# Performance work log

Hardware: AMD Instinct MI355X
Metric: run time of the kernel (lower is better)

Reference implementation:

```python
import jax, jax.numpy as jnp
import numpy as np

BS, RAL, LAL = 128, 1024, 256
CS, VOC, HFS, EMB = 256, 34, 512, 256


def setup_inputs() -> dict:
    key0 = jax.random.key(0)
    ks = jax.random.split(key0, 16)
    s = 0.02
    # mask from random valid lengths (at least 1 valid frame per example)
    lengths = jax.random.randint(ks[15], (BS,), RAL // 2, RAL + 1)
    mask = (jnp.arange(RAL)[None, :] < lengths[:, None]).astype(jnp.float32)
    return {
        "key": jax.random.normal(ks[0], (BS, RAL, CS), jnp.float32),
        "val": jax.random.normal(ks[1], (BS, RAL, CS), jnp.float32),
        "mask": mask,
        "emb": jax.random.normal(ks[2], (VOC, EMB), jnp.float32) * s,
        "Wih_a": jax.random.normal(ks[3], (4 * HFS, EMB + CS), jnp.float32) * s,
        "Whh_a": jax.random.normal(ks[4], (4 * HFS, HFS), jnp.float32) * s,
        "bih_a": jnp.zeros((4 * HFS,), jnp.float32),
        "bhh_a": jnp.zeros((4 * HFS,), jnp.float32),
        "Wih_b": jax.random.normal(ks[5], (4 * HFS, HFS), jnp.float32) * s,
        "Whh_b": jax.random.normal(ks[6], (4 * HFS, HFS), jnp.float32) * s,
        "bih_b": jnp.zeros((4 * HFS,), jnp.float32),
        "bhh_b": jnp.zeros((4 * HFS,), jnp.float32),
        "Wq": jax.random.normal(ks[7], (CS, HFS), jnp.float32) * s,
        "bq": jnp.zeros((CS,), jnp.float32),
        "Wc": jax.random.normal(ks[8], (VOC, HFS + CS), jnp.float32) * s,
        "bc": jnp.zeros((VOC,), jnp.float32),
        "y": jax.random.randint(ks[9], (BS, LAL), 0, VOC, jnp.int32),
    }


def _lstm_cell(x, h, c, Wih, Whh, bih, bhh):
    z = x @ Wih.T + bih + h @ Whh.T + bhh  # (BS, 4H)
    i, f, g, o = jnp.split(z, 4, axis=-1)
    i, f, o = jax.nn.sigmoid(i), jax.nn.sigmoid(f), jax.nn.sigmoid(o)
    g = jnp.tanh(g)
    c2 = f * c + i * g
    return o * jnp.tanh(c2), c2


def _attend(key, val, query, mask):
    # energy: (BS, RAL) = bmm(key, query[...,None])
    energy = jnp.einsum("brc,bc->br", key, query)
    att = jax.nn.softmax(energy, axis=1) * mask
    att = att / jnp.sum(att, axis=1, keepdims=True)
    return jnp.einsum("br,brc->bc", att, val)  # context (BS, CS)


def reference(key, val, mask, emb, Wih_a, Whh_a, bih_a, bhh_a,
              Wih_b, Whh_b, bih_b, bhh_b, Wq, bq, Wc, bc, y):
    bs = y.shape[0]
    z = jnp.zeros((bs, HFS), jnp.float32)
    init = (z, z, z, z, jnp.zeros((bs, CS), jnp.float32))

    def step(carry, y_t):
        ha, ca, hb, cb, ctx = carry
        e = emb[y_t]  # (BS, EMB)
        x = jnp.concatenate([e, ctx], axis=1)
        ha, ca = _lstm_cell(x, ha, ca, Wih_a, Whh_a, bih_a, bhh_a)
        hb, cb = _lstm_cell(ha, hb, cb, Wih_b, Whh_b, bih_b, bhh_b)
        query = hb @ Wq.T + bq  # (BS, CS)
        ctx = _attend(key, val, query, mask)
        logits = jnp.concatenate([hb, ctx], axis=1) @ Wc.T + bc  # (BS, VOC)
        return (ha, ca, hb, cb, ctx), logits

    _, preds = jax.lax.scan(step, init, y.T)  # (LAL, BS, VOC)
    return jnp.transpose(preds, (1, 0, 2))  # (BS, LAL, VOC)
```

## Files before the change

kernel.cpp:

```cpp
#include <hip/hip_runtime.h>
#include <cstdint>
#include <cstddef>

static constexpr int BS  = 128;
static constexpr int RAL = 1024;
static constexpr int LAL = 256;
static constexpr int CS  = 256;
static constexpr int VOC = 34;
static constexpr int HFS = 512;
static constexpr int EMB = 256;

static constexpr int NSPLIT = 2;
static constexpr int RSPL   = RAL / NSPLIT;

typedef float  f32x4  __attribute__((ext_vector_type(4)));
typedef short  bf16x8 __attribute__((ext_vector_type(8)));

static __device__ __forceinline__ float bflo(unsigned int u) {
    return __builtin_bit_cast(float, u << 16);
}
static __device__ __forceinline__ float bfhi(unsigned int u) {
    return __builtin_bit_cast(float, u & 0xffff0000u);
}
static __device__ __forceinline__ unsigned short f2bf(float f) {
    unsigned int x = __builtin_bit_cast(unsigned int, f);
    x = (x + 0x7fffu + ((x >> 16) & 1u)) >> 16;
    return (unsigned short)x;
}
static __device__ __forceinline__ float sigf(float x)   { return 1.0f / (1.0f + __expf(-x)); }
static __device__ __forceinline__ float tanhf_(float x) { return 1.0f - 2.0f / (__expf(2.0f * x) + 1.0f); }

__global__ void cvt4_kernel(const float4* __restrict__ in, ushort4* __restrict__ out, int n4) {
    int i  = blockIdx.x * blockDim.x + threadIdx.x;
    int st = gridDim.x * blockDim.x;
    for (; i < n4; i += st) {
        float4 v = in[i];
        ushort4 o;
        o.x = f2bf(v.x); o.y = f2bf(v.y); o.z = f2bf(v.z); o.w = f2bf(v.w);
        out[i] = o;
    }
}

__global__ __launch_bounds__(256) void len_kernel(const float* __restrict__ mask, int* __restrict__ Llen) {
    __shared__ int red[256];
    const int b = blockIdx.x, tid = threadIdx.x;
    int c = 0;
    for (int r = tid; r < RAL; r += 256) c += (mask[b * RAL + r] != 0.0f) ? 1 : 0;
    red[tid] = c;
    __syncthreads();
    for (int s = 128; s > 0; s >>= 1) {
        if (tid < s) red[tid] += red[tid + s];
        __syncthreads();
    }
    if (tid == 0) Llen[b] = red[0];
}

__global__ __launch_bounds__(256) void lstm_kernel(
    const unsigned short* __restrict__ p0, int s0,
    const unsigned short* __restrict__ p1, int s1,
    const unsigned short* __restrict__ p2, int s2,
    const unsigned short* __restrict__ p3, int s3,
    const int* __restrict__ yidx, int t,
    const unsigned short* __restrict__ Wih, const unsigned short* __restrict__ Whh,
    const float* __restrict__ bih, const float* __restrict__ bhh,
    float* __restrict__ cst,
    unsigned short* __restrict__ hout)
{
    __shared__ __align__(16) float zp[3][4][64][4];

    const int tid  = threadIdx.x;
    const int lane = tid & 63;
    const int wv   = tid >> 6;
    const int quad = lane >> 4;
    const int l16  = lane & 15;
    const int j    = blockIdx.x * 16 + l16;
    const int mrow = blockIdx.y * 16 + l16;

    const unsigned short* pa;
    const unsigned short* wb;
    {
        const unsigned short* const ps[4] = {p0, p1, p2, p3};
        const int ss[4] = {s0, s1, s2, s3};
        long rbase;
        if (wv == 0 && yidx) rbase = (long)yidx[mrow * LAL + t] * ss[0];
        else                 rbase = (long)mrow * ss[wv];
        pa = ps[wv] + rbase + quad * 8;
        const unsigned short* Wp = (wv < 2) ? Wih : Whh;
        wb = Wp + (wv & 1) * 256 + quad * 8;
    }

    const unsigned short* wg[4];
#pragma unroll
    for (int g = 0; g < 4; ++g) wg[g] = wb + (long)(g * HFS + j) * HFS;

    f32x4 acc[4];
#pragma unroll
    for (int g = 0; g < 4; ++g) acc[g] = (f32x4)0.0f;

#pragma unroll
    for (int kc = 0; kc < 8; ++kc) {
        bf16x8 a  = *(const bf16x8*)(pa + kc * 32);
        bf16x8 b0 = *(const bf16x8*)(wg[0] + kc * 32);
        bf16x8 b1 = *(const bf16x8*)(wg[1] + kc * 32);
        bf16x8 b2 = *(const bf16x8*)(wg[2] + kc * 32);
        bf16x8 b3 = *(const bf16x8*)(wg[3] + kc * 32);
        acc[0] = __builtin_amdgcn_mfma_f32_16x16x32_bf16(a, b0, acc[0], 0, 0, 0);
        acc[1] = __builtin_amdgcn_mfma_f32_16x16x32_bf16(a, b1, acc[1], 0, 0, 0);
        acc[2] = __builtin_amdgcn_mfma_f32_16x16x32_bf16(a, b2, acc[2], 0, 0, 0);
        acc[3] = __builtin_amdgcn_mfma_f32_16x16x32_bf16(a, b3, acc[3], 0, 0, 0);
    }

    if (wv != 0) {
#pragma unroll
        for (int g = 0; g < 4; ++g)
            *(f32x4*)&zp[wv - 1][g][lane][0] = acc[g];
    }
    __syncthreads();
    if (wv == 0) {
#pragma unroll
        for (int g = 0; g < 4; ++g) {
            acc[g] += *(const f32x4*)&zp[0][g][lane][0];
            acc[g] += *(const f32x4*)&zp[1][g][lane][0];
            acc[g] += *(const f32x4*)&zp[2][g][lane][0];
        }
        const float bI = bih[j]           + bhh[j];
        const float bF = bih[HFS + j]     + bhh[HFS + j];
        const float bG = bih[2 * HFS + j] + bhh[2 * HFS + j];
        const float bO = bih[3 * HFS + j] + bhh[3 * HFS + j];
#pragma unroll
        for (int r = 0; r < 4; ++r) {
            int m   = blockIdx.y * 16 + quad * 4 + r;
            int idx = m * HFS + j;
            float iv = sigf(acc[0][r] + bI);
            float fv = sigf(acc[1][r] + bF);
            float gv = tanhf_(acc[2][r] + bG);
            float ov = sigf(acc[3][r] + bO);
            float cn = fv * cst[idx] + iv * gv;
            cst[idx] = cn;
            hout[idx] = f2bf(ov * tanhf_(cn));
        }
    }
}

template <bool KVBF>
__global__ __launch_bounds__(1024) void attn_part_kernel(
    const void* __restrict__ keyp, const void* __restrict__ valp,
    const int* __restrict__ Llen,
    const unsigned short* __restrict__ hbv,
    const unsigned short* __restrict__ Wqb,
    const float* __restrict__ bq,
    float* __restrict__ attM, float* __restrict__ attS,
    float* __restrict__ attC)
{
    __shared__ __align__(16) float hb_l[HFS];
    __shared__ __align__(16) float q_lds[CS];
    __shared__ __align__(16) float e_lds[RSPL];
    __shared__ __align__(16) float ctxp[16][CS];
    __shared__ float red[32];

    const int tid   = threadIdx.x;
    const int b     = blockIdx.x;
    const int sp    = blockIdx.y;
    const int L     = Llen[b];
    const int rbase = sp * RSPL;
    int nv = L - rbase;
    if (nv > RSPL) nv = RSPL;

    if (nv <= 0) {
        if (tid < CS) attC[((long)b * NSPLIT + sp) * CS + tid] = 0.0f;
        if (tid == 0) { attM[b * NSPLIT + sp] = -1e30f; attS[b * NSPLIT + sp] = 0.0f; }
        return;
    }

    if (tid < HFS) hb_l[tid] = bflo((unsigned int)hbv[b * HFS + tid]);
    __syncthreads();

    {
        const int c  = tid >> 2;
        const int jj = tid & 3;
        const unsigned short* wr = Wqb + (long)c * HFS + jj * 128;
        const float* xr = &hb_l[jj * 128];
        float qa = 0.0f;
#pragma unroll
        for (int k = 0; k < 128; k += 8) {
            uint4 u = *(const uint4*)(wr + k);
            float4 h0 = *(const float4*)(xr + k);
            float4 h1 = *(const float4*)(xr + k + 4);
            qa += bflo(u.x) * h0.x + bfhi(u.x) * h0.y
                + bflo(u.y) * h0.z + bfhi(u.y) * h0.w
                + bflo(u.z) * h1.x + bfhi(u.z) * h1.y
                + bflo(u.w) * h1.z + bfhi(u.w) * h1.w;
        }
        qa += __shfl_xor(qa, 1);
        qa += __shfl_xor(qa, 2);
        if (jj == 0) q_lds[c] = qa + bq[c];
    }
    __syncthreads();

    {
        const int jj   = tid & 7;
        const int rloc = tid >> 3;
        for (int r0 = 0; r0 < nv; r0 += 128) {
            const int r = r0 + rloc;
            float acc = 0.0f;
            if (r < nv) {
                if (KVBF) {
                    const unsigned short* kp = (const unsigned short*)keyp
                        + ((long)b * RAL + rbase + r) * CS + jj * 32;
#pragma unroll
                    for (int i = 0; i < 4; ++i) {
                        uint4 u = *(const uint4*)(kp + i * 8);
                        const float* qp = &q_lds[jj * 32 + i * 8];
                        float4 qa  = *(const float4*)qp;
                        float4 qb2 = *(const float4*)(qp + 4);
                        acc += bflo(u.x) * qa.x  + bfhi(u.x) * qa.y
                             + bflo(u.y) * qa.z  + bfhi(u.y) * qa.w
                             + bflo(u.z) * qb2.x + bfhi(u.z) * qb2.y
                             + bflo(u.w) * qb2.z + bfhi(u.w) * qb2.w;
                    }
                } else {
                    const float* kp = (const float*)keyp
                        + ((long)b * RAL + rbase + r) * CS + jj * 32;
#pragma unroll
                    for (int i = 0; i < 8; ++i) {
                        float4 kv = *(const float4*)(kp + i * 4);
                        float4 qa = *(const float4*)&q_lds[jj * 32 + i * 4];
                        acc += kv.x * qa.x + kv.y * qa.y + kv.z * qa.z + kv.w * qa.w;
                    }
                }
            }
            acc += __shfl_xor(acc, 1);
            acc += __shfl_xor(acc, 2);
            acc += __shfl_xor(acc, 4);
            if (jj == 0 && r < nv) e_lds[r] = acc;
        }
    }
    __syncthreads();

    float pm = (tid < nv) ? e_lds[tid] : -1e30f;
#pragma unroll
    for (int s = 32; s > 0; s >>= 1) pm = fmaxf(pm, __shfl_xor(pm, s));
    if ((tid & 63) == 0) red[tid >> 6] = pm;
    __syncthreads();
    float M = red[0];
#pragma unroll
    for (int i = 1; i < 16; ++i) M = fmaxf(M, red[i]);

    float ps = 0.0f;
    if (tid < nv) { float v = __expf(e_lds[tid] - M); e_lds[tid] = v; ps = v; }
#pragma unroll
    for (int s = 32; s > 0; s >>= 1) ps += __shfl_xor(ps, s);
    if ((tid & 63) == 0) red[16 + (tid >> 6)] = ps;
    __syncthreads();
    float S = 0.0f;
#pragma unroll
    for (int i = 0; i < 16; ++i) S += red[16 + i];

    if (tid == 0) { attM[b * NSPLIT + sp] = M; attS[b * NSPLIT + sp] = S; }

    {
        const int wv = tid >> 6;
        const int c4 = (tid & 63) * 4;
        float a0 = 0.f, a1 = 0.f, a2 = 0.f, a3 = 0.f;
        if (KVBF) {
            const unsigned short* vb = (const unsigned short*)valp
                + ((long)b * RAL + rbase) * CS + c4;
            int r = wv;
            for (; r + 48 < nv; r += 64) {
                uint2 u0 = *(const uint2*)(vb + (long)(r)      * CS);
                uint2 u1 = *(const uint2*)(vb + (long)(r + 16) * CS);
                uint2 u2 = *(const uint2*)(vb + (long)(r + 32) * CS);
                uint2 u3 = *(const uint2*)(vb + (long)(r + 48) * CS);
                float w0 = e_lds[r], w1 = e_lds[r + 16], w2 = e_lds[r + 32], w3 = e_lds[r + 48];
                a0 += w0 * bflo(u0.x) + w1 * bflo(u1.x) + w2 * bflo(u2.x) + w3 * bflo(u3.x);
                a1 += w0 * bfhi(u0.x) + w1 * bfhi(u1.x) + w2 * bfhi(u2.x) + w3 * bfhi(u3.x);
                a2 += w0 * bflo(u0.y) + w1 * bflo(u1.y) + w2 * bflo(u2.y) + w3 * bflo(u3.y);
                a3 += w0 * bfhi(u0.y) + w1 * bfhi(u1.y) + w2 * bfhi(u2.y) + w3 * bfhi(u3.y);
            }
            for (; r < nv; r += 16) {
                uint2 u = *(const uint2*)(vb + (long)r * CS);
                float w = e_lds[r];
                a0 += w * bflo(u.x); a1 += w * bfhi(u.x);
                a2 += w * bflo(u.y); a3 += w * bfhi(u.y);
            }
        } else {
            const float* vb = (const float*)valp + ((long)b * RAL + rbase) * CS + c4;
            int r = wv;
            for (; r + 48 < nv; r += 64) {
                float4 v0 = *(const float4*)(vb + (long)(r)      * CS);
                float4 v1 = *(const float4*)(vb + (long)(r + 16) * CS);
                float4 v2 = *(const float4*)(vb + (long)(r + 32) * CS);
                float4 v3 = *(const float4*)(vb + (long)(r + 48) * CS);
                float w0 = e_lds[r], w1 = e_lds[r + 16], w2 = e_lds[r + 32], w3 = e_lds[r + 48];
                a0 += w0 * v0.x + w1 * v1.x + w2 * v2.x + w3 * v3.x;
                a1 += w0 * v0.y + w1 * v1.y + w2 * v2.y + w3 * v3.y;
                a2 += w0 * v0.z + w1 * v1.z + w2 * v2.z + w3 * v3.z;
                a3 += w0 * v0.w + w1 * v1.w + w2 * v2.w + w3 * v3.w;
            }
            for (; r < nv; r += 16) {
                float4 v = *(const float4*)(vb + (long)r * CS);
                float w = e_lds[r];
                a0 += w * v.x; a1 += w * v.y; a2 += w * v.z; a3 += w * v.w;
            }
        }
        float4 out4 = {a0, a1, a2, a3};
        *(float4*)&ctxp[tid >> 6][c4] = out4;
    }
    __syncthreads();

    if (tid < CS) {
        float cv = 0.0f;
#pragma unroll
        for (int w = 0; w < 16; ++w) cv += ctxp[w][tid];
        attC[((long)b * NSPLIT + sp) * CS + tid] = cv;
    }
}

__global__ __launch_bounds__(512) void attn_comb_kernel(
    const float* __restrict__ attM, const float* __restrict__ attS,
    const float* __restrict__ attC,
    const unsigned short* __restrict__ hbv,
    const float* __restrict__ Wc, const float* __restrict__ bc,
    unsigned short* __restrict__ ctxbf,
    float* __restrict__ outp, int t)
{
    __shared__ __align__(16) float xcat[HFS + CS];
    __shared__ float wsc[NSPLIT];

    const int tid = threadIdx.x;
    const int b   = blockIdx.x;

    if (tid == 0) {
        float M = attM[b * NSPLIT];
#pragma unroll
        for (int s = 1; s < NSPLIT; ++s) M = fmaxf(M, attM[b * NSPLIT + s]);
        float S = 0.0f;
        float w[NSPLIT];
#pragma unroll
        for (int s = 0; s < NSPLIT; ++s) {
            w[s] = __expf(attM[b * NSPLIT + s] - M);
            S += w[s] * attS[b * NSPLIT + s];
        }
        const float invS = 1.0f / S;
#pragma unroll
        for (int s = 0; s < NSPLIT; ++s) wsc[s] = w[s] * invS;
    }
    if (tid < HFS) xcat[tid] = bflo((unsigned int)hbv[b * HFS + tid]);
    __syncthreads();

    if (tid < CS) {
        float cv = 0.0f;
#pragma unroll
        for (int s = 0; s < NSPLIT; ++s)
            cv += wsc[s] * attC[((long)b * NSPLIT + s) * CS + tid];
        xcat[HFS + tid] = cv;
        ctxbf[b * CS + tid] = f2bf(cv);
    }
    __syncthreads();

    if (tid < VOC * 8) {
        const int v   = tid >> 3;
        const int jj2 = tid & 7;
        const float* wr = Wc + (long)v * (HFS + CS) + jj2 * 96;
        const float* xr = &xcat[jj2 * 96];
        float part = 0.0f;
#pragma unroll
        for (int i = 0; i < 24; ++i) {
            float4 wv4 = *(const float4*)(wr + i * 4);
            float4 xv  = *(const float4*)(xr + i * 4);
            part += wv4.x * xv.x + wv4.y * xv.y + wv4.z * xv.z + wv4.w * xv.w;
        }
        part += __shfl_xor(part, 1);
        part += __shfl_xor(part, 2);
        part += __shfl_xor(part, 4);
        if (jj2 == 0)
            outp[((long)b * LAL + t) * VOC + v] = part + bc[v];
    }
}

extern "C" void kernel_launch(void* const* d_in, const int* in_sizes, int n_in,
                              void* d_out, int out_size, void* d_ws, size_t ws_size,
                              hipStream_t stream)
{
    (void)in_sizes; (void)n_in; (void)out_size;
    const float* keyf  = (const float*)d_in[0];
    const float* valf  = (const float*)d_in[1];
    const float* mask  = (const float*)d_in[2];
    const float* embf  = (const float*)d_in[3];
    const float* WihAf = (const float*)d_in[4];
    const float* WhhAf = (const float*)d_in[5];
    const float* bihA  = (const float*)d_in[6];
    const float* bhhA  = (const float*)d_in[7];
    const float* WihBf = (const float*)d_in[8];
    const float* WhhBf = (const float*)d_in[9];
    const float* bihB  = (const float*)d_in[10];
    const float* bhhB  = (const float*)d_in[11];
    const float* Wqf   = (const float*)d_in[12];
    const float* bq    = (const float*)d_in[13];
    const float* Wc    = (const float*)d_in[14];
    const float* bc    = (const float*)d_in[15];
    const int*   y     = (const int*)d_in[16];
    float* outp = (float*)d_out;

    size_t off = 0;
    auto take = [&](size_t bytes) -> void* {
        void* p = (char*)d_ws + off;
        off += (bytes + 255) & ~(size_t)255;
        return p;
    };

    unsigned short* ha    = (unsigned short*)take((size_t)2 * BS * HFS * 2);
    unsigned short* hbuf  = (unsigned short*)take((size_t)2 * BS * HFS * 2);
    float*          ca    = (float*)take((size_t)BS * HFS * 4);
    float*          cbuf  = (float*)take((size_t)BS * HFS * 4);
    unsigned short* ctxbf = (unsigned short*)take((size_t)BS * CS * 2);
    size_t stateBytes = off;

    int*            Llen  = (int*)take((size_t)BS * 4);
    unsigned short* embb  = (unsigned short*)take((size_t)VOC * EMB * 2);
    unsigned short* WihAb = (unsigned short*)take((size_t)4 * HFS * HFS * 2);
    unsigned short* WhhAb = (unsigned short*)take((size_t)4 * HFS * HFS * 2);
    unsigned short* WihBb = (unsigned short*)take((size_t)4 * HFS * HFS * 2);
    unsigned short* WhhBb = (unsigned short*)take((size_t)4 * HFS * HFS * 2);
    unsigned short* Wqb   = (unsigned short*)take((size_t)CS * HFS * 2);

    float* attM = (float*)take((size_t)BS * NSPLIT * 4);
    float* attS = (float*)take((size_t)BS * NSPLIT * 4);
    float* attC = (float*)take((size_t)BS * NSPLIT * CS * 4);

    const size_t kvBytes = (size_t)BS * RAL * CS * 2;
    unsigned short* keyb = nullptr;
    unsigned short* valb = nullptr;
    bool kvbf = false;
    bool keyInVal = false;
    if (off + 2 * (kvBytes + 256) <= ws_size) {
        keyb = (unsigned short*)take(kvBytes);
        valb = (unsigned short*)take(kvBytes);
        kvbf = true;
    } else if (off + kvBytes + 256 <= ws_size) {
        valb = (unsigned short*)take(kvBytes);
        keyb = (unsigned short*)d_in[1];
        kvbf = true;
        keyInVal = true;
    }

    hipMemsetAsync(d_ws, 0, stateBytes, stream);
    len_kernel<<<dim3(BS), dim3(256), 0, stream>>>(mask, Llen);

    auto cvt = [&](const float* src, unsigned short* dst, long n) {
        int n4 = (int)(n / 4);
        int blocks = (n4 + 255) / 256;
        if (blocks > 8192) blocks = 8192;
        cvt4_kernel<<<dim3(blocks), dim3(256), 0, stream>>>((const float4*)src, (ushort4*)dst, n4);
    };
    cvt(embf,  embb,  (long)VOC * EMB);
    cvt(WihAf, WihAb, (long)4 * HFS * HFS);
    cvt(WhhAf, WhhAb, (long)4 * HFS * HFS);
    cvt(WihBf, WihBb, (long)4 * HFS * HFS);
    cvt(WhhBf, WhhBb, (long)4 * HFS * HFS);
    cvt(Wqf,   Wqb,   (long)CS * HFS);
    if (kvbf) {
        if (keyInVal) {
            cvt(valf, valb, (long)BS * RAL * CS);
            cvt(keyf, keyb, (long)BS * RAL * CS);
        } else {
            cvt(keyf, keyb, (long)BS * RAL * CS);
            cvt(valf, valb, (long)BS * RAL * CS);
        }
    }

    for (int t = 0; t < LAL; ++t) {
        unsigned short* haIn  = ha   + (t & 1) * (BS * HFS);
        unsigned short* haOut = ha   + ((t + 1) & 1) * (BS * HFS);
        unsigned short* hbIn  = hbuf + (t & 1) * (BS * HFS);
        unsigned short* hbOut = hbuf + ((t + 1) & 1) * (BS * HFS);

        lstm_kernel<<<dim3(32, 8), dim3(256), 0, stream>>>(
            embb, EMB, ctxbf, CS, haIn, HFS, haIn + 256, HFS,
            y, t, WihAb, WhhAb, bihA, bhhA, ca, haOut);

        lstm_kernel<<<dim3(32, 8), dim3(256), 0, stream>>>(
            haOut, HFS, haOut + 256, HFS, hbIn, HFS, hbIn + 256, HFS,
            nullptr, t, WihBb, WhhBb, bihB, bhhB, cbuf, hbOut);

        if (kvbf)
            attn_part_kernel<true><<<dim3(BS, NSPLIT), dim3(1024), 0, stream>>>(
                keyb, valb, Llen, hbOut, Wqb, bq, attM, attS, attC);
        else
            attn_part_kernel<false><<<dim3(BS, NSPLIT), dim3(1024), 0, stream>>>(
                keyf, valf, Llen, hbOut, Wqb, bq, attM, attS, attC);

        attn_comb_kernel<<<dim3(BS), dim3(512), 0, stream>>>(
            attM, attS, attC, hbOut, Wc, bc, ctxbf, outp, t);
    }
}
```

Baseline: 12.77 ms.

## Fuse per-timestep kernels into one cooperative persistent kernel with grid syncs

Replaces the four kernel launches per decoder step (1024 launches total) with one cooperative persistent kernel of 256 blocks x 512 threads, using grid.sync between the LSTM, attention and combine phases. Each phase is remapped to the new block and thread shape: LSTM splits K across 8 waves, and attention uses 512 threads. Attention now splits the valid length evenly between the two halves instead of at the fixed midpoint, which balances the work. The aim is to remove launch overhead, at the cost of four grid-wide barriers per step and lower occupancy.

```diff
diff --git a/kernel.cpp b/kernel.cpp
--- a/kernel.cpp
+++ b/kernel.cpp
@@ -1,6 +1,9 @@
 #include <hip/hip_runtime.h>
+#include <hip/hip_cooperative_groups.h>
 #include <cstdint>
 #include <cstddef>
+
+namespace cg = cooperative_groups;
 
 static constexpr int BS  = 128;
 static constexpr int RAL = 1024;
@@ -55,39 +58,76 @@
     if (tid == 0) Llen[b] = red[0];
 }
 
-__global__ __launch_bounds__(256) void lstm_kernel(
-    const unsigned short* __restrict__ p0, int s0,
-    const unsigned short* __restrict__ p1, int s1,
-    const unsigned short* __restrict__ p2, int s2,
-    const unsigned short* __restrict__ p3, int s3,
-    const int* __restrict__ yidx, int t,
-    const unsigned short* __restrict__ Wih, const unsigned short* __restrict__ Whh,
-    const float* __restrict__ bih, const float* __restrict__ bhh,
-    float* __restrict__ cst,
-    unsigned short* __restrict__ hout)
+struct SmLstm { float zp[7][4][64][4]; };
+struct SmAttn {
+    float hb_l[HFS];
+    float q_lds[CS];
+    float e_lds[RSPL];
+    float ctxp[8][CS];
+    float red[16];
+};
+struct SmComb {
+    float xcat[HFS + CS];
+    float wsc[NSPLIT];
+};
+static constexpr size_t SMSZ =
+    sizeof(SmLstm) > sizeof(SmAttn)
+        ? (sizeof(SmLstm) > sizeof(SmComb) ? sizeof(SmLstm) : sizeof(SmComb))
+        : (sizeof(SmAttn) > sizeof(SmComb) ? sizeof(SmAttn) : sizeof(SmComb));
+
+struct PParams {
+    const void* keyp; const void* valp;
+    const int* Llen; const int* y;
+    const unsigned short* embb;
+    const unsigned short* WihA; const unsigned short* WhhA;
+    const float* bihA; const float* bhhA;
+    const unsigned short* WihB; const unsigned short* WhhB;
+    const float* bihB; const float* bhhB;
+    const unsigned short* Wqb; const float* bq;
+    const float* Wc; const float* bc;
+    unsigned short* ha; unsigned short* hbuf;
+    float* ca; float* cbuf;
+    unsigned short* ctxbf;
+    float* attM; float* attS; float* attC;
+    float* outp;
+};
+
+static __device__ __forceinline__ void lstm_phase(
+    int blk, int tid,
+    const unsigned short* p0, int s0,
+    const unsigned short* p1, int s1,
+    const unsigned short* p2, int s2,
+    const unsigned short* p3, int s3,
+    const int* yidx, int t,
+    const unsigned short* Wih, const unsigned short* Whh,
+    const float* bih, const float* bhh,
+    float* cst, unsigned short* hout,
+    SmLstm* sm)
 {
-    __shared__ __align__(16) float zp[3][4][64][4];
-
-    const int tid  = threadIdx.x;
     const int lane = tid & 63;
     const int wv   = tid >> 6;
+    const int seg  = wv >> 1;
+    const int sub  = wv & 1;
     const int quad = lane >> 4;
     const int l16  = lane & 15;
-    const int j    = blockIdx.x * 16 + l16;
-    const int mrow = blockIdx.y * 16 + l16;
-
-    const unsigned short* pa;
-    const unsigned short* wb;
-    {
-        const unsigned short* const ps[4] = {p0, p1, p2, p3};
-        const int ss[4] = {s0, s1, s2, s3};
-        long rbase;
-        if (wv == 0 && yidx) rbase = (long)yidx[mrow * LAL + t] * ss[0];
-        else                 rbase = (long)mrow * ss[wv];
-        pa = ps[wv] + rbase + quad * 8;
-        const unsigned short* Wp = (wv < 2) ? Wih : Whh;
-        wb = Wp + (wv & 1) * 256 + quad * 8;
-    }
+    const int jsl  = blk & 31;
+    const int bgr  = blk >> 5;
+    const int j    = jsl * 16 + l16;
+    const int mrow = bgr * 16 + l16;
+
+    const unsigned short* base;
+    int stride;
+    if      (seg == 0) { base = p0; stride = s0; }
+    else if (seg == 1) { base = p1; stride = s1; }
+    else if (seg == 2) { base = p2; stride = s2; }
+    else               { base = p3; stride = s3; }
+
+    long rbase;
+    if (seg == 0 && yidx) rbase = (long)yidx[mrow * LAL + t] * stride;
+    else                  rbase = (long)mrow * stride;
+
+    const unsigned short* pa = base + rbase + sub * 128 + quad * 8;
+    const unsigned short* wb = ((seg < 2) ? Wih : Whh) + (seg & 1) * 256 + sub * 128 + quad * 8;
 
     const unsigned short* wg[4];
 #pragma unroll
@@ -98,7 +138,7 @@
     for (int g = 0; g < 4; ++g) acc[g] = (f32x4)0.0f;
 
 #pragma unroll
-    for (int kc = 0; kc < 8; ++kc) {
+    for (int kc = 0; kc < 4; ++kc) {
         bf16x8 a  = *(const bf16x8*)(pa + kc * 32);
         bf16x8 b0 = *(const bf16x8*)(wg[0] + kc * 32);
         bf16x8 b1 = *(const bf16x8*)(wg[1] + kc * 32);
@@ -113,15 +153,15 @@
     if (wv != 0) {
 #pragma unroll
         for (int g = 0; g < 4; ++g)
-            *(f32x4*)&zp[wv - 1][g][lane][0] = acc[g];
+            *(f32x4*)&sm->zp[wv - 1][g][lane][0] = acc[g];
     }
     __syncthreads();
     if (wv == 0) {
 #pragma unroll
         for (int g = 0; g < 4; ++g) {
-            acc[g] += *(const f32x4*)&zp[0][g][lane][0];
-            acc[g] += *(const f32x4*)&zp[1][g][lane][0];
-            acc[g] += *(const f32x4*)&zp[2][g][lane][0];
+#pragma unroll
+            for (int w = 0; w < 7; ++w)
+                acc[g] += *(const f32x4*)&sm->zp[w][g][lane][0];
         }
         const float bI = bih[j]           + bhh[j];
         const float bF = bih[HFS + j]     + bhh[HFS + j];
@@ -129,7 +169,7 @@
         const float bO = bih[3 * HFS + j] + bhh[3 * HFS + j];
 #pragma unroll
         for (int r = 0; r < 4; ++r) {
-            int m   = blockIdx.y * 16 + quad * 4 + r;
+            int m   = bgr * 16 + quad * 4 + r;
             int idx = m * HFS + j;
             float iv = sigf(acc[0][r] + bI);
             float fv = sigf(acc[1][r] + bF);
@@ -143,28 +183,22 @@
 }
 
 template <bool KVBF>
-__global__ __launch_bounds__(1024) void attn_part_kernel(
-    const void* __restrict__ keyp, const void* __restrict__ valp,
+static __device__ __forceinline__ void attn_phase(
+    int blk, int tid,
+    const void* keyp, const void* valp,
     const int* __restrict__ Llen,
     const unsigned short* __restrict__ hbv,
-    const unsigned short* __restrict__ Wqb,
-    const float* __restrict__ bq,
-    float* __restrict__ attM, float* __restrict__ attS,
-    float* __restrict__ attC)
+    const unsigned short* __restrict__ Wqb, const float* __restrict__ bq,
+    float* __restrict__ attM, float* __restrict__ attS, float* __restrict__ attC,
+    SmAttn* sm)
 {
-    __shared__ __align__(16) float hb_l[HFS];
-    __shared__ __align__(16) float q_lds[CS];
-    __shared__ __align__(16) float e_lds[RSPL];
-    __shared__ __align__(16) float ctxp[16][CS];
-    __shared__ float red[32];
-
-    const int tid   = threadIdx.x;
-    const int b     = blockIdx.x;
-    const int sp    = blockIdx.y;
+    const int b     = blk >> 1;
+    const int sp    = blk & 1;
     const int L     = Llen[b];
-    const int rbase = sp * RSPL;
+    const int rhalf = (L + 1) >> 1;
+    const int rbase = sp * rhalf;
     int nv = L - rbase;
-    if (nv > RSPL) nv = RSPL;
+    if (nv > rhalf) nv = rhalf;
 
     if (nv <= 0) {
         if (tid < CS) attC[((long)b * NSPLIT + sp) * CS + tid] = 0.0f;
@@ -172,17 +206,17 @@
         return;
     }
 
-    if (tid < HFS) hb_l[tid] = bflo((unsigned int)hbv[b * HFS + tid]);
+    sm->hb_l[tid] = bflo((unsigned int)hbv[b * HFS + tid]);
     __syncthreads();
 
     {
-        const int c  = tid >> 2;
-        const int jj = tid & 3;
-        const unsigned short* wr = Wqb + (long)c * HFS + jj * 128;
-        const float* xr = &hb_l[jj * 128];
+        const int c  = tid >> 1;
+        const int jj = tid & 1;
+        const unsigned short* wr = Wqb + (long)c * HFS + jj * 256;
+        const float* xr = &sm->hb_l[jj * 256];
         float qa = 0.0f;
-#pragma unroll
-        for (int k = 0; k < 128; k += 8) {
+#pragma unroll 8
+        for (int k = 0; k < 256; k += 8) {
             uint4 u = *(const uint4*)(wr + k);
             float4 h0 = *(const float4*)(xr + k);
             float4 h1 = *(const float4*)(xr + k + 4);
@@ -192,15 +226,14 @@
                 + bflo(u.w) * h1.z + bfhi(u.w) * h1.w;
         }
         qa += __shfl_xor(qa, 1);
-        qa += __shfl_xor(qa, 2);
-        if (jj == 0) q_lds[c] = qa + bq[c];
+        if (jj == 0) sm->q_lds[c] = qa + bq[c];
     }
     __syncthreads();
 
     {
         const int jj   = tid & 7;
         const int rloc = tid >> 3;
-        for (int r0 = 0; r0 < nv; r0 += 128) {
+        for (int r0 = 0; r0 < nv; r0 += 64) {
             const int r = r0 + rloc;
             float acc = 0.0f;
             if (r < nv) {
@@ -210,7 +243,7 @@
 #pragma unroll
                     for (int i = 0; i < 4; ++i) {
                         uint4 u = *(const uint4*)(kp + i * 8);
-                        const float* qp = &q_lds[jj * 32 + i * 8];
+                        const float* qp = &sm->q_lds[jj * 32 + i * 8];
                         float4 qa  = *(const float4*)qp;
                         float4 qb2 = *(const float4*)(qp + 4);
                         acc += bflo(u.x) * qa.x  + bfhi(u.x) * qa.y
@@ -224,7 +257,7 @@
 #pragma unroll
                     for (int i = 0; i < 8; ++i) {
                         float4 kv = *(const float4*)(kp + i * 4);
-                        float4 qa = *(const float4*)&q_lds[jj * 32 + i * 4];
+                        float4 qa = *(const float4*)&sm->q_lds[jj * 32 + i * 4];
                         acc += kv.x * qa.x + kv.y * qa.y + kv.z * qa.z + kv.w * qa.w;
                     }
                 }
@@ -232,29 +265,29 @@
             acc += __shfl_xor(acc, 1);
             acc += __shfl_xor(acc, 2);
             acc += __shfl_xor(acc, 4);
-            if (jj == 0 && r < nv) e_lds[r] = acc;
-        }
-    }
-    __syncthreads();
-
-    float pm = (tid < nv) ? e_lds[tid] : -1e30f;
+            if (jj == 0 && r < nv) sm->e_lds[r] = acc;
+        }
+    }
+    __syncthreads();
+
+    float pm = (tid < nv) ? sm->e_lds[tid] : -1e30f;
 #pragma unroll
     for (int s = 32; s > 0; s >>= 1) pm = fmaxf(pm, __shfl_xor(pm, s));
-    if ((tid & 63) == 0) red[tid >> 6] = pm;
-    __syncthreads();
-    float M = red[0];
-#pragma unroll
-    for (int i = 1; i < 16; ++i) M = fmaxf(M, red[i]);
+    if ((tid & 63) == 0) sm->red[tid >> 6] = pm;
+    __syncthreads();
+    float M = sm->red[0];
+#pragma unroll
+    for (int i = 1; i < 8; ++i) M = fmaxf(M, sm->red[i]);
 
     float ps = 0.0f;
-    if (tid < nv) { float v = __expf(e_lds[tid] - M); e_lds[tid] = v; ps = v; }
+    if (tid < nv) { float v = __expf(sm->e_lds[tid] - M); sm->e_lds[tid] = v; ps = v; }
 #pragma unroll
     for (int s = 32; s > 0; s >>= 1) ps += __shfl_xor(ps, s);
-    if ((tid & 63) == 0) red[16 + (tid >> 6)] = ps;
+    if ((tid & 63) == 0) sm->red[8 + (tid >> 6)] = ps;
     __syncthreads();
     float S = 0.0f;
 #pragma unroll
-    for (int i = 0; i < 16; ++i) S += red[16 + i];
+    for (int i = 0; i < 8; ++i) S += sm->red[8 + i];
 
     if (tid == 0) { attM[b * NSPLIT + sp] = M; attS[b * NSPLIT + sp] = S; }
 
@@ -266,70 +299,68 @@
             const unsigned short* vb = (const unsigned short*)valp
                 + ((long)b * RAL + rbase) * CS + c4;
             int r = wv;
-            for (; r + 48 < nv; r += 64) {
+            for (; r + 24 < nv; r += 32) {
                 uint2 u0 = *(const uint2*)(vb + (long)(r)      * CS);
-                uint2 u1 = *(const uint2*)(vb + (long)(r + 16) * CS);
-                uint2 u2 = *(const uint2*)(vb + (long)(r + 32) * CS);
-                uint2 u3 = *(const uint2*)(vb + (long)(r + 48) * CS);
-                float w0 = e_lds[r], w1 = e_lds[r + 16], w2 = e_lds[r + 32], w3 = e_lds[r + 48];
+                uint2 u1 = *(const uint2*)(vb + (long)(r + 8)  * CS);
+                uint2 u2 = *(const uint2*)(vb + (long)(r + 16) * CS);
+                uint2 u3 = *(const uint2*)(vb + (long)(r + 24) * CS);
+                float w0 = sm->e_lds[r],      w1 = sm->e_lds[r + 8];
+                float w2 = sm->e_lds[r + 16], w3 = sm->e_lds[r + 24];
                 a0 += w0 * bflo(u0.x) + w1 * bflo(u1.x) + w2 * bflo(u2.x) + w3 * bflo(u3.x);
                 a1 += w0 * bfhi(u0.x) + w1 * bfhi(u1.x) + w2 * bfhi(u2.x) + w3 * bfhi(u3.x);
                 a2 += w0 * bflo(u0.y) + w1 * bflo(u1.y) + w2 * bflo(u2.y) + w3 * bflo(u3.y);
                 a3 += w0 * bfhi(u0.y) + w1 * bfhi(u1.y) + w2 * bfhi(u2.y) + w3 * bfhi(u3.y);
             }
-            for (; r < nv; r += 16) {
+            for (; r < nv; r += 8) {
                 uint2 u = *(const uint2*)(vb + (long)r * CS);
-                float w = e_lds[r];
+                float w = sm->e_lds[r];
                 a0 += w * bflo(u.x); a1 += w * bfhi(u.x);
                 a2 += w * bflo(u.y); a3 += w * bfhi(u.y);
             }
         } else {
             const float* vb = (const float*)valp + ((long)b * RAL + rbase) * CS + c4;
             int r = wv;
-            for (; r + 48 < nv; r += 64) {
+            for (; r + 24 < nv; r += 32) {
                 float4 v0 = *(const float4*)(vb + (long)(r)      * CS);
-                float4 v1 = *(const float4*)(vb + (long)(r + 16) * CS);
-                float4 v2 = *(const float4*)(vb + (long)(r + 32) * CS);
-                float4 v3 = *(const float4*)(vb + (long)(r + 48) * CS);
-                float w0 = e_lds[r], w1 = e_lds[r + 16], w2 = e_lds[r + 32], w3 = e_lds[r + 48];
+                float4 v1 = *(const float4*)(vb + (long)(r + 8)  * CS);
+                float4 v2 = *(const float4*)(vb + (long)(r + 16) * CS);
+                float4 v3 = *(const float4*)(vb + (long)(r + 24) * CS);
+                float w0 = sm->e_lds[r],      w1 = sm->e_lds[r + 8];
+                float w2 = sm->e_lds[r + 16], w3 = sm->e_lds[r + 24];
                 a0 += w0 * v0.x + w1 * v1.x + w2 * v2.x + w3 * v3.x;
                 a1 += w0 * v0.y + w1 * v1.y + w2 * v2.y + w3 * v3.y;
                 a2 += w0 * v0.z + w1 * v1.z + w2 * v2.z + w3 * v3.z;
                 a3 += w0 * v0.w + w1 * v1.w + w2 * v2.w + w3 * v3.w;
             }
-            for (; r < nv; r += 16) {
+            for (; r < nv; r += 8) {
                 float4 v = *(const float4*)(vb + (long)r * CS);
-                float w = e_lds[r];
+                float w = sm->e_lds[r];
                 a0 += w * v.x; a1 += w * v.y; a2 += w * v.z; a3 += w * v.w;
             }
         }
         float4 out4 = {a0, a1, a2, a3};
-        *(float4*)&ctxp[tid >> 6][c4] = out4;
+        *(float4*)&sm->ctxp[tid >> 6][c4] = out4;
     }
     __syncthreads();
 
     if (tid < CS) {
         float cv = 0.0f;
 #pragma unroll
-        for (int w = 0; w < 16; ++w) cv += ctxp[w][tid];
+        for (int w = 0; w < 8; ++w) cv += sm->ctxp[w][tid];
         attC[((long)b * NSPLIT + sp) * CS + tid] = cv;
     }
 }
 
-__global__ __launch_bounds__(512) void attn_comb_kernel(
+static __device__ __forceinline__ void comb_phase(
+    int b, int tid,
     const float* __restrict__ attM, const float* __restrict__ attS,
     const float* __restrict__ attC,
     const unsigned short* __restrict__ hbv,
     const float* __restrict__ Wc, const float* __restrict__ bc,
     unsigned short* __restrict__ ctxbf,
-    float* __restrict__ outp, int t)
+    float* __restrict__ outp, int t,
+    SmComb* sm)
 {
-    __shared__ __align__(16) float xcat[HFS + CS];
-    __shared__ float wsc[NSPLIT];
-
-    const int tid = threadIdx.x;
-    const int b   = blockIdx.x;
-
     if (tid == 0) {
         float M = attM[b * NSPLIT];
 #pragma unroll
@@ -343,17 +374,17 @@
         }
         const float invS = 1.0f / S;
 #pragma unroll
-        for (int s = 0; s < NSPLIT; ++s) wsc[s] = w[s] * invS;
-    }
-    if (tid < HFS) xcat[tid] = bflo((unsigned int)hbv[b * HFS + tid]);
+        for (int s = 0; s < NSPLIT; ++s) sm->wsc[s] = w[s] * invS;
+    }
+    sm->xcat[tid] = bflo((unsigned int)hbv[b * HFS + tid]);
     __syncthreads();
 
     if (tid < CS) {
         float cv = 0.0f;
 #pragma unroll
         for (int s = 0; s < NSPLIT; ++s)
-            cv += wsc[s] * attC[((long)b * NSPLIT + s) * CS + tid];
-        xcat[HFS + tid] = cv;
+            cv += sm->wsc[s] * attC[((long)b * NSPLIT + s) * CS + tid];
+        sm->xcat[HFS + tid] = cv;
         ctxbf[b * CS + tid] = f2bf(cv);
     }
     __syncthreads();
@@ -362,7 +393,7 @@
         const int v   = tid >> 3;
         const int jj2 = tid & 7;
         const float* wr = Wc + (long)v * (HFS + CS) + jj2 * 96;
-        const float* xr = &xcat[jj2 * 96];
+        const float* xr = &sm->xcat[jj2 * 96];
         float part = 0.0f;
 #pragma unroll
         for (int i = 0; i < 24; ++i) {
@@ -375,6 +406,45 @@
         part += __shfl_xor(part, 4);
         if (jj2 == 0)
             outp[((long)b * LAL + t) * VOC + v] = part + bc[v];
+    }
+}
+
+template <bool KVBF>
+__global__ __launch_bounds__(512, 2) void persist_kernel(PParams P)
+{
+    cg::grid_group grid = cg::this_grid();
+    __shared__ __align__(16) unsigned char smraw[SMSZ];
+    SmLstm* smL = (SmLstm*)smraw;
+    SmAttn* smA = (SmAttn*)smraw;
+    SmComb* smC = (SmComb*)smraw;
+
+    const int blk = blockIdx.x;
+    const int tid = threadIdx.x;
+
+    for (int t = 0; t < LAL; ++t) {
+        unsigned short* haIn  = P.ha   + (t & 1) * (BS * HFS);
+        unsigned short* haOut = P.ha   + ((t + 1) & 1) * (BS * HFS);
+        unsigned short* hbIn  = P.hbuf + (t & 1) * (BS * HFS);
+        unsigned short* hbOut = P.hbuf + ((t + 1) & 1) * (BS * HFS);
+
+        lstm_phase(blk, tid,
+                   P.embb, EMB, P.ctxbf, CS, haIn, HFS, haIn + 256, HFS,
+                   P.y, t, P.WihA, P.WhhA, P.bihA, P.bhhA, P.ca, haOut, smL);
+        grid.sync();
+
+        lstm_phase(blk, tid,
+                   haOut, HFS, haOut + 256, HFS, hbIn, HFS, hbIn + 256, HFS,
+                   nullptr, t, P.WihB, P.WhhB, P.bihB, P.bhhB, P.cbuf, hbOut, smL);
+        grid.sync();
+
+        attn_phase<KVBF>(blk, tid, P.keyp, P.valp, P.Llen, hbOut,
+                         P.Wqb, P.bq, P.attM, P.attS, P.attC, smA);
+        grid.sync();
+
+        if (blk < BS)
+            comb_phase(blk, tid, P.attM, P.attS, P.attC, hbOut,
+                       P.Wc, P.bc, P.ctxbf, P.outp, t, smC);
+        grid.sync();
     }
 }
 
@@ -469,28 +539,24 @@
         }
     }
 
-    for (int t = 0; t < LAL; ++t) {
-        unsigned short* haIn  = ha   + (t & 1) * (BS * HFS);
-        unsigned short* haOut = ha   + ((t + 1) & 1) * (BS * HFS);
-        unsigned short* hbIn  = hbuf + (t & 1) * (BS * HFS);
-        unsigned short* hbOut = hbuf + ((t + 1) & 1) * (BS * HFS);
-
-        lstm_kernel<<<dim3(32, 8), dim3(256), 0, stream>>>(
-            embb, EMB, ctxbf, CS, haIn, HFS, haIn + 256, HFS,
-            y, t, WihAb, WhhAb, bihA, bhhA, ca, haOut);
-
-        lstm_kernel<<<dim3(32, 8), dim3(256), 0, stream>>>(
-            haOut, HFS, haOut + 256, HFS, hbIn, HFS, hbIn + 256, HFS,
-            nullptr, t, WihBb, WhhBb, bihB, bhhB, cbuf, hbOut);
-
-        if (kvbf)
-            attn_part_kernel<true><<<dim3(BS, NSPLIT), dim3(1024), 0, stream>>>(
-                keyb, valb, Llen, hbOut, Wqb, bq, attM, attS, attC);
-        else
-            attn_part_kernel<false><<<dim3(BS, NSPLIT), dim3(1024), 0, stream>>>(
-                keyf, valf, Llen, hbOut, Wqb, bq, attM, attS, attC);
-
-        attn_comb_kernel<<<dim3(BS), dim3(512), 0, stream>>>(
-            attM, attS, attC, hbOut, Wc, bc, ctxbf, outp, t);
-    }
-}
+    PParams prm;
+    prm.keyp = kvbf ? (const void*)keyb : (const void*)keyf;
+    prm.valp = kvbf ? (const void*)valb : (const void*)valf;
+    prm.Llen = Llen; prm.y = y;
+    prm.embb = embb;
+    prm.WihA = WihAb; prm.WhhA = WhhAb; prm.bihA = bihA; prm.bhhA = bhhA;
+    prm.WihB = WihBb; prm.WhhB = WhhBb; prm.bihB = bihB; prm.bhhB = bhhB;
+    prm.Wqb = Wqb; prm.bq = bq; prm.Wc = Wc; prm.bc = bc;
+    prm.ha = ha; prm.hbuf = hbuf; prm.ca = ca; prm.cbuf = cbuf;
+    prm.ctxbf = ctxbf;
+    prm.attM = attM; prm.attS = attS; prm.attC = attC;
+    prm.outp = outp;
+
+    void* kargs[] = { &prm };
+    if (kvbf)
+        hipLaunchCooperativeKernel(reinterpret_cast<void*>(&persist_kernel<true>),
+                                   dim3(256), dim3(512), kargs, 0, stream);
+    else
+        hipLaunchCooperativeKernel(reinterpret_cast<void*>(&persist_kernel<false>),
+                                   dim3(256), dim3(512), kargs, 0, stream);
+}
```

New measurement: 40.37 ms. 3.16x slower.
